# Performance work log

Measured on AMD Instinct MI355X. Metric: run time of the kernel, lower is better.

Reference implementation:

```python
import jax, jax.numpy as jnp
import numpy as np

N, C, H, W = 2, 128, 64, 256
GROUPS, S = 8, 9  # 3x3 search window


def setup_inputs() -> dict:
    key = jax.random.key(0)
    k1, k2, k3 = jax.random.split(key, 3)
    left = jax.random.normal(k1, (N, C, H, W), jnp.float32)
    right = jax.random.normal(k2, (N, C, H, W), jnp.float32)
    # per-pixel learned offsets: (N, S*2, H, W), reshaped to (N,S,2,H,W) inside
    extra_offset = jax.random.normal(k3, (N, S * 2, H, W), jnp.float32)
    return {"left_feature": left, "right_feature": right, "extra_offset": extra_offset}


def _bilinear_sample(im, x, y):
    """im: (N,C,H,W); x,y: (N,L) pixel coords. Zero padding outside borders
    (matches bilinear_grid_sample: 1-px zero pad + index clamp into pad)."""
    n, c, h, w = im.shape
    x0f = jnp.floor(x)
    y0f = jnp.floor(y)
    x1f = x0f + 1.0
    y1f = y0f + 1.0
    wa = (x1f - x) * (y1f - y)
    wb = (x1f - x) * (y - y0f)
    wc = (x - x0f) * (y1f - y)
    wd = (x - x0f) * (y - y0f)
    ph, pw = h + 2, w + 2
    im_p = jnp.pad(im, ((0, 0), (0, 0), (1, 1), (1, 1))).reshape(n, c, ph * pw)
    x0 = jnp.clip(x0f.astype(jnp.int32) + 1, 0, pw - 1)
    x1 = jnp.clip(x1f.astype(jnp.int32) + 1, 0, pw - 1)
    y0 = jnp.clip(y0f.astype(jnp.int32) + 1, 0, ph - 1)
    y1 = jnp.clip(y1f.astype(jnp.int32) + 1, 0, ph - 1)

    def g(xi, yi):
        idx = (xi + yi * pw)[:, None, :]  # (N,1,L) -> broadcast over C
        return jnp.take_along_axis(im_p, idx, axis=2)

    out = (g(x0, y0) * wa[:, None, :] + g(x0, y1) * wb[:, None, :]
           + g(x1, y0) * wc[:, None, :] + g(x1, y1) * wd[:, None, :])
    return out  # (N,C,L)


def reference(left_feature, right_feature, extra_offset):
    n, c, h, w = left_feature.shape
    cg = c // GROUPS
    # base 3x3 offsets, (x,y) pairs in torch meshgrid 'ij' order
    r = jnp.arange(-1, 2, dtype=jnp.float32)
    xg, yg = jnp.meshgrid(r, r, indexing='ij')
    base = jnp.stack([xg, yg], axis=-1).reshape(S, 2)  # (9,2)
    eo = extra_offset.reshape(n, S, 2, h, w).transpose(0, 1, 3, 4, 2)  # (N,S,H,W,2)
    off = base[None, :, None, None, :] + eo
    gx = jnp.arange(w, dtype=jnp.float32)
    gy = jnp.arange(h, dtype=jnp.float32)
    x = (off[..., 0] + gx[None, None, None, :]).reshape(n, -1)  # (N, S*H*W)
    y = (off[..., 1] + gy[None, None, :, None]).reshape(n, -1)
    # offsets are shared across groups -> sample all channels once
    sampled = _bilinear_sample(right_feature, x, y).reshape(n, GROUPS, cg, S, h, w)
    left_g = left_feature.reshape(n, GROUPS, cg, 1, h, w)
    corr = jnp.mean(left_g * sampled, axis=2)  # (N, GROUPS, S, H, W)
    return corr.reshape(n, GROUPS * S, h, w)
```

## Files before the change

kernel.cpp:

```cpp
#include <hip/hip_runtime.h>
#include <stdint.h>


#define NB 2
#define CC 128
#define HH 64
#define WW 256
#define GG 8
#define CG 16
#define SS 9
#define HW (HH * WW)
#define TY 4
#define RW 5
#define NSLOT 16
#define HALFDW 1056
#define SLOTQ (2 * HALFDW)
#define SMEMDW (NSLOT * SLOTQ)

typedef __fp16 h2v __attribute__((ext_vector_type(2)));

static __device__ __forceinline__ uint32_t pkrtz(float a, float b) {
    h2v v = __builtin_amdgcn_cvt_pkrtz(a, b);
    return __builtin_bit_cast(uint32_t, v);
}
static __device__ __forceinline__ h2v u2h(uint32_t u) {
    return __builtin_bit_cast(h2v, u);
}

#if __has_builtin(__builtin_amdgcn_fdot2)
#define FDOT2(A, B, C) __builtin_amdgcn_fdot2((A), (B), (C), false)
#else
#define FDOT2(A, B, C) fmaf((float)(A).x, (float)(B).x, \
                            fmaf((float)(A).y, (float)(B).y, (C)))
#endif

#define DOT16(LOP, RES)                                                        \
  {                                                                            \
    const uint4 u0_ = *(const uint4*)(LOP);                                    \
    const uint4 u1_ = *(const uint4*)((LOP) + HALFDW);                         \
    RES = FDOT2(u2h(u0_.x), u2h(lvpk[0]),                                      \
          FDOT2(u2h(u0_.y), u2h(lvpk[1]),                                      \
          FDOT2(u2h(u0_.z), u2h(lvpk[2]),                                      \
          FDOT2(u2h(u0_.w), u2h(lvpk[3]),                                      \
          FDOT2(u2h(u1_.x), u2h(lvpk[4]),                                      \
          FDOT2(u2h(u1_.y), u2h(lvpk[5]),                                      \
          FDOT2(u2h(u1_.z), u2h(lvpk[6]),                                      \
          FDOT2(u2h(u1_.w), u2h(lvpk[7]), 0.0f))))))));                        \
  }

__global__ __launch_bounds__(1024) void corr_kernel(
    const float* __restrict__ left, const float* __restrict__ right,
    const float* __restrict__ eo, float* __restrict__ out)
{
    __shared__ uint32_t smem[SMEMDW];

    const int tid = threadIdx.x;
    const int lane = tid & 63;
    const int wv = tid >> 6;
    const int bid = blockIdx.x;
    const int g = bid & (GG - 1);
    const int h0 = ((bid >> 3) & 15) << 2;
    const int n = bid >> 7;
    const int gch = g * CG;

    const int virt_row0 = h0 - RW;
    const int row0 = max(0, virt_row0);
    const int row_last = min(HH - 1, h0 + TY + RW - 1);
    const int nrows = row_last - row0 + 1;
    const int sbase = row0 - virt_row0 + 1;

    const int hh = tid >> 8;
    const int h = h0 + hh;
    const int wcol = tid & 255;
    const int pix = h * WW + wcol;

    const float* rnb = right + (size_t)n * CC * HW;
    const float* lp  = left  + (size_t)(n * CC + gch) * HW + pix;
    const float* eob = eo + (size_t)n * SS * 2 * HW + pix;

    {
        const bool staged = (wv >= sbase) && (wv < sbase + nrows);
        uint32_t* slot = &smem[wv * SLOTQ];
        if (!staged) {
            for (int i = lane; i < SLOTQ / 4; i += 64)
                *(uint4*)&slot[4 * i] = make_uint4(0u, 0u, 0u, 0u);
        } else if (lane < 16) {
            const int half = lane >> 3;
            const int cellsel = (lane >> 2) & 1;
            const int dwi = lane & 3;
            slot[half * HALFDW + cellsel * (257 * 4) + dwi] = 0u;
        }
    }

    float eox[SS], eoy[SS];
#pragma unroll
    for (int s = 0; s < SS; ++s) {
        eox[s] = eob[(2 * s) * HW];
        eoy[s] = eob[(2 * s + 1) * HW];
    }

    __syncthreads();

#pragma unroll
    for (int pass = 0; pass < 4; ++pass) {
        if (wv < nrows) {
            const int cq = 64 * pass + lane;
            const float* s0 = rnb + (size_t)gch * HW + (row0 + wv) * WW + cq;
            uint32_t pk8[8];
#pragma unroll
            for (int p = 0; p < 8; ++p)
                pk8[p] = pkrtz(s0[(size_t)(2 * p) * HW],
                               s0[(size_t)(2 * p + 1) * HW]);
            uint32_t* dst = &smem[(sbase + wv) * SLOTQ + 4 * (cq + 1)];
            *(uint4*)dst            = make_uint4(pk8[0], pk8[1], pk8[2], pk8[3]);
            *(uint4*)(dst + HALFDW) = make_uint4(pk8[4], pk8[5], pk8[6], pk8[7]);
        }
    }

    uint32_t lvpk[8];
#pragma unroll
    for (int p = 0; p < 8; ++p)
        lvpk[p] = pkrtz(lp[(size_t)(2 * p) * HW], lp[(size_t)(2 * p + 1) * HW]);

    float acc[SS];
#pragma unroll
    for (int s = 0; s < SS; ++s) acc[s] = 0.0f;

    __syncthreads();

#pragma unroll
    for (int s = 0; s < SS; ++s) {
        const float x = (float)(s / 3 - 1) + eox[s] + (float)wcol;
        const float y = (float)(s % 3 - 1) + eoy[s] + (float)h;
        const float x0f = floorf(x), y0f = floorf(y);
        const float fx0 = x - x0f, fx1 = 1.0f - fx0;
        const float fy0 = y - y0f, fy1 = 1.0f - fy0;
        const int x0 = (int)x0f, y0 = (int)y0f;
        const int x1 = x0 + 1,   y1 = y0 + 1;
        const bool vx0 = (unsigned)x0 < (unsigned)WW;
        const bool vx1 = (unsigned)x1 < (unsigned)WW;
        const bool vy0 = (unsigned)y0 < (unsigned)HH;
        const bool vy1 = (unsigned)y1 < (unsigned)HH;
        const float wA = (vx0 && vy0) ? fx1 * fy1 : 0.0f;
        const float wB = (vx1 && vy0) ? fx0 * fy1 : 0.0f;
        const float wC = (vx0 && vy1) ? fx1 * fy0 : 0.0f;
        const float wD = (vx1 && vy1) ? fx0 * fy0 : 0.0f;

        const bool bad = (vy0 && (y0 < row0 || y0 > row_last)) ||
                         (vy1 && (y1 < row0 || y1 > row_last));

        if (__builtin_expect(!bad, 1)) {
            const int xc = min(max(x0, -1), WW);
            const int rr = min(max(y0 - virt_row0 + 1, 0), NSLOT - 2);
            const uint32_t* rp0 = smem + rr * SLOTQ + 4 * (xc + 1);
            const uint32_t* rp1 = rp0 + SLOTQ;
            float dA, dB, dC, dD;
            DOT16(rp0,     dA)
            DOT16(rp0 + 4, dB)
            DOT16(rp1,     dC)
            DOT16(rp1 + 4, dD)
            acc[s] += fmaf(wA, dA, fmaf(wB, dB, fmaf(wC, dC, wD * dD)));
        } else {
            const int cx0 = min(max(x0, 0), WW - 1), cx1 = min(max(x1, 0), WW - 1);
            const int cy0 = min(max(y0, 0), HH - 1), cy1 = min(max(y1, 0), HH - 1);
#pragma unroll
            for (int p = 0; p < 8; ++p) {
                const h2v lv = u2h(lvpk[p]);
#pragma unroll
                for (int c2 = 0; c2 < 2; ++c2) {
                    const float* rp2 = rnb + (size_t)(gch + 2 * p + c2) * HW;
                    const float v = wA * rp2[cy0 * WW + cx0] + wB * rp2[cy0 * WW + cx1]
                                  + wC * rp2[cy1 * WW + cx0] + wD * rp2[cy1 * WW + cx1];
                    acc[s] += (c2 ? (float)lv.y : (float)lv.x) * v;
                }
            }
        }
    }

    float* ob = out + ((size_t)(n * GG + g) * SS) * HW + pix;
#pragma unroll
    for (int s = 0; s < SS; ++s)
        ob[s * HW] = acc[s] * (1.0f / CG);
}

extern "C" void kernel_launch(void* const* d_in, const int* in_sizes, int n_in,
                              void* d_out, int out_size, void* d_ws, size_t ws_size,
                              hipStream_t stream) {
    const float* left  = (const float*)d_in[0];
    const float* right = (const float*)d_in[1];
    const float* eo    = (const float*)d_in[2];
    float* out = (float*)d_out;
    (void)d_ws; (void)ws_size; (void)in_sizes; (void)n_in; (void)out_size;

    dim3 grid(NB * (HH / TY) * GG);
    dim3 block(1024);
    corr_kernel<<<grid, block, 0, stream>>>(left, right, eo, out);
}
```

Baseline: 21.00 us.

## Split width into halves and channels across thread pairs with LDS reduction

The grid now tiles the width into two 128-column halves, doubling the block count. Each pixel is handled by two threads that each cover 8 of the 16 group channels, and their partial sums are combined through shared memory before the store. The shared-memory slot shrinks to a 140-cell window with halo, and samples that fall outside that window now take the global-memory fallback path. This trades an extra reduction barrier and wider halo staging for more blocks, smaller LDS use and fewer registers per thread.

```diff
diff --git a/kernel.cpp b/kernel.cpp
--- a/kernel.cpp
+++ b/kernel.cpp
@@ -11,10 +11,13 @@
 #define SS 9
 #define HW (HH * WW)
 #define TY 4
+#define WT 128
 #define RW 5
 #define NSLOT 16
-#define HALFDW 1056
-#define SLOTQ (2 * HALFDW)
+#define NCELL 140
+#define CELL0 6
+#define HALF 560
+#define SLOTQ (2 * HALF)
 #define SMEMDW (NSLOT * SLOTQ)
 
 typedef __fp16 h2v __attribute__((ext_vector_type(2)));
@@ -34,18 +37,13 @@
                             fmaf((float)(A).y, (float)(B).y, (C)))
 #endif
 
-#define DOT16(LOP, RES)                                                        \
+#define DOT8(P, RES)                                                           \
   {                                                                            \
-    const uint4 u0_ = *(const uint4*)(LOP);                                    \
-    const uint4 u1_ = *(const uint4*)((LOP) + HALFDW);                         \
-    RES = FDOT2(u2h(u0_.x), u2h(lvpk[0]),                                      \
-          FDOT2(u2h(u0_.y), u2h(lvpk[1]),                                      \
-          FDOT2(u2h(u0_.z), u2h(lvpk[2]),                                      \
-          FDOT2(u2h(u0_.w), u2h(lvpk[3]),                                      \
-          FDOT2(u2h(u1_.x), u2h(lvpk[4]),                                      \
-          FDOT2(u2h(u1_.y), u2h(lvpk[5]),                                      \
-          FDOT2(u2h(u1_.z), u2h(lvpk[6]),                                      \
-          FDOT2(u2h(u1_.w), u2h(lvpk[7]), 0.0f))))))));                        \
+    const uint4 u_ = *(const uint4*)(P);                                       \
+    RES = FDOT2(u2h(u_.x), u2h(lvpk[0]),                                       \
+          FDOT2(u2h(u_.y), u2h(lvpk[1]),                                       \
+          FDOT2(u2h(u_.z), u2h(lvpk[2]),                                       \
+          FDOT2(u2h(u_.w), u2h(lvpk[3]), 0.0f))));                             \
   }
 
 __global__ __launch_bounds__(1024) void corr_kernel(
@@ -58,10 +56,12 @@
     const int lane = tid & 63;
     const int wv = tid >> 6;
     const int bid = blockIdx.x;
-    const int g = bid & (GG - 1);
-    const int h0 = ((bid >> 3) & 15) << 2;
-    const int n = bid >> 7;
+    const int g = bid & 7;
+    const int wh = (bid >> 3) & 1;
+    const int h0 = ((bid >> 4) & 15) << 2;
+    const int n = bid >> 8;
     const int gch = g * CG;
+    const int wbase = wh * WT;
 
     const int virt_row0 = h0 - RW;
     const int row0 = max(0, virt_row0);
@@ -69,26 +69,23 @@
     const int nrows = row_last - row0 + 1;
     const int sbase = row0 - virt_row0 + 1;
 
+    const int wcol7 = tid & 127;
+    const int chh = (tid >> 7) & 1;
     const int hh = tid >> 8;
     const int h = h0 + hh;
-    const int wcol = tid & 255;
+    const int wcol = wbase + wcol7;
     const int pix = h * WW + wcol;
 
     const float* rnb = right + (size_t)n * CC * HW;
-    const float* lp  = left  + (size_t)(n * CC + gch) * HW + pix;
+    const float* lp  = left  + (size_t)(n * CC + gch + chh * 8) * HW + pix;
     const float* eob = eo + (size_t)n * SS * 2 * HW + pix;
 
     {
         const bool staged = (wv >= sbase) && (wv < sbase + nrows);
-        uint32_t* slot = &smem[wv * SLOTQ];
         if (!staged) {
+            uint32_t* slot = &smem[wv * SLOTQ];
             for (int i = lane; i < SLOTQ / 4; i += 64)
                 *(uint4*)&slot[4 * i] = make_uint4(0u, 0u, 0u, 0u);
-        } else if (lane < 16) {
-            const int half = lane >> 3;
-            const int cellsel = (lane >> 2) & 1;
-            const int dwi = lane & 3;
-            slot[half * HALFDW + cellsel * (257 * 4) + dwi] = 0u;
         }
     }
 
@@ -101,25 +98,33 @@
 
     __syncthreads();
 
-#pragma unroll
-    for (int pass = 0; pass < 4; ++pass) {
-        if (wv < nrows) {
-            const int cq = 64 * pass + lane;
-            const float* s0 = rnb + (size_t)gch * HW + (row0 + wv) * WW + cq;
-            uint32_t pk8[8];
-#pragma unroll
-            for (int p = 0; p < 8; ++p)
-                pk8[p] = pkrtz(s0[(size_t)(2 * p) * HW],
-                               s0[(size_t)(2 * p + 1) * HW]);
-            uint32_t* dst = &smem[(sbase + wv) * SLOTQ + 4 * (cq + 1)];
-            *(uint4*)dst            = make_uint4(pk8[0], pk8[1], pk8[2], pk8[3]);
-            *(uint4*)(dst + HALFDW) = make_uint4(pk8[4], pk8[5], pk8[6], pk8[7]);
+    if (wv < nrows) {
+        const float* rowp = rnb + (size_t)gch * HW + (row0 + wv) * WW;
+        uint32_t* slotp = &smem[(sbase + wv) * SLOTQ];
+#pragma unroll
+        for (int pass = 0; pass < 3; ++pass) {
+            const int cell = pass * 64 + lane;
+            if (cell < NCELL) {
+                const int gcol = wbase + cell - CELL0;
+                const bool vc = (unsigned)gcol < (unsigned)WW;
+                uint32_t pk8[8];
+#pragma unroll
+                for (int p = 0; p < 8; ++p) {
+                    const float a = vc ? rowp[(size_t)(2 * p) * HW + gcol] : 0.0f;
+                    const float b = vc ? rowp[(size_t)(2 * p + 1) * HW + gcol] : 0.0f;
+                    pk8[p] = pkrtz(a, b);
+                }
+                *(uint4*)&slotp[4 * cell] =
+                    make_uint4(pk8[0], pk8[1], pk8[2], pk8[3]);
+                *(uint4*)&slotp[HALF + 4 * cell] =
+                    make_uint4(pk8[4], pk8[5], pk8[6], pk8[7]);
+            }
         }
     }
 
-    uint32_t lvpk[8];
-#pragma unroll
-    for (int p = 0; p < 8; ++p)
+    uint32_t lvpk[4];
+#pragma unroll
+    for (int p = 0; p < 4; ++p)
         lvpk[p] = pkrtz(lp[(size_t)(2 * p) * HW], lp[(size_t)(2 * p + 1) * HW]);
 
     float acc[SS];
@@ -146,41 +151,57 @@
         const float wC = (vx0 && vy1) ? fx1 * fy0 : 0.0f;
         const float wD = (vx1 && vy1) ? fx0 * fy0 : 0.0f;
 
-        const bool bad = (vy0 && (y0 < row0 || y0 > row_last)) ||
-                         (vy1 && (y1 < row0 || y1 > row_last));
+        const bool bad =
+            (vy0 && (y0 < row0 || y0 > row_last)) ||
+            (vy1 && (y1 < row0 || y1 > row_last)) ||
+            (vx0 && (x0 < wbase - CELL0)) ||
+            (vx1 && (x1 > wbase + NCELL - CELL0 - 1));
 
         if (__builtin_expect(!bad, 1)) {
-            const int xc = min(max(x0, -1), WW);
+            const int xcell = min(max(x0 - wbase + CELL0, 0), NCELL - 2);
             const int rr = min(max(y0 - virt_row0 + 1, 0), NSLOT - 2);
-            const uint32_t* rp0 = smem + rr * SLOTQ + 4 * (xc + 1);
-            const uint32_t* rp1 = rp0 + SLOTQ;
+            const uint32_t* b0 = smem + rr * SLOTQ + chh * HALF + 4 * xcell;
+            const uint32_t* b1 = b0 + SLOTQ;
             float dA, dB, dC, dD;
-            DOT16(rp0,     dA)
-            DOT16(rp0 + 4, dB)
-            DOT16(rp1,     dC)
-            DOT16(rp1 + 4, dD)
-            acc[s] += fmaf(wA, dA, fmaf(wB, dB, fmaf(wC, dC, wD * dD)));
+            DOT8(b0,     dA)
+            DOT8(b0 + 4, dB)
+            DOT8(b1,     dC)
+            DOT8(b1 + 4, dD)
+            acc[s] = fmaf(wA, dA, fmaf(wB, dB, fmaf(wC, dC, wD * dD)));
         } else {
             const int cx0 = min(max(x0, 0), WW - 1), cx1 = min(max(x1, 0), WW - 1);
             const int cy0 = min(max(y0, 0), HH - 1), cy1 = min(max(y1, 0), HH - 1);
-#pragma unroll
-            for (int p = 0; p < 8; ++p) {
+            float val = 0.0f;
+#pragma unroll
+            for (int p = 0; p < 4; ++p) {
                 const h2v lv = u2h(lvpk[p]);
 #pragma unroll
                 for (int c2 = 0; c2 < 2; ++c2) {
-                    const float* rp2 = rnb + (size_t)(gch + 2 * p + c2) * HW;
+                    const float* rp2 =
+                        rnb + (size_t)(gch + chh * 8 + 2 * p + c2) * HW;
                     const float v = wA * rp2[cy0 * WW + cx0] + wB * rp2[cy0 * WW + cx1]
                                   + wC * rp2[cy1 * WW + cx0] + wD * rp2[cy1 * WW + cx1];
-                    acc[s] += (c2 ? (float)lv.y : (float)lv.x) * v;
+                    val += (c2 ? (float)lv.y : (float)lv.x) * v;
                 }
             }
+            acc[s] = val;
         }
     }
 
-    float* ob = out + ((size_t)(n * GG + g) * SS) * HW + pix;
-#pragma unroll
-    for (int s = 0; s < SS; ++s)
-        ob[s * HW] = acc[s] * (1.0f / CG);
+    __syncthreads();
+    if (chh == 1) {
+        float* cs = (float*)smem + (hh * WT + wcol7) * SS;
+#pragma unroll
+        for (int s = 0; s < SS; ++s) cs[s] = acc[s];
+    }
+    __syncthreads();
+    if (chh == 0) {
+        const float* cs = (const float*)smem + (hh * WT + wcol7) * SS;
+        float* ob = out + ((size_t)(n * GG + g) * SS) * HW + pix;
+#pragma unroll
+        for (int s = 0; s < SS; ++s)
+            ob[s * HW] = (acc[s] + cs[s]) * (1.0f / CG);
+    }
 }
 
 extern "C" void kernel_launch(void* const* d_in, const int* in_sizes, int n_in,
@@ -192,7 +213,7 @@
     float* out = (float*)d_out;
     (void)d_ws; (void)ws_size; (void)in_sizes; (void)n_in; (void)out_size;
 
-    dim3 grid(NB * (HH / TY) * GG);
-    dim3 block(1024);
+    dim3 grid(NB * (HH / TY) * (WW / WT) * GG);
+    dim3 block(TY * WT * 2);
     corr_kernel<<<grid, block, 0, stream>>>(left, right, eo, out);
 }
```

Result: slower. 27.85 us (+32.7%).
